# Performance work log

Measured on AMD Instinct MI355X. Metric: run time of the kernel, lower is better.

Reference implementation:

```python
import jax, jax.numpy as jnp
import numpy as np

N = 50000

def gcn_conv(x, W, b, src, dst, n):
    # x: [N, Fin], W: [Fin, Fout]; PyG GCNConv: transform then sym-normalized aggregate (self-loops included in src/dst)
    h = x @ W  # [N, Fout]
    deg = jax.ops.segment_sum(jnp.ones_like(dst, dtype=h.dtype), dst, num_segments=n)
    inv_sqrt = jnp.where(deg > 0, jax.lax.rsqrt(deg), 0.0)
    norm = inv_sqrt[src] * inv_sqrt[dst]  # [E+N]
    msg = h[src] * norm[:, None]
    out = jax.ops.segment_sum(msg, dst, num_segments=n)
    return out + b


def setup_inputs() -> dict:
    key = jax.random.key(0)
    ks = jax.random.split(key, 8)
    d_in, d_h, n_exp, E = 64, 64, 16, 800000
    x = jax.random.normal(ks[0], (N, d_in), dtype=jnp.float32)
    edge_index = jax.random.randint(ks[1], (2, E), 0, N, dtype=jnp.int64)
    s = 1.0 / np.sqrt(d_in)
    W1 = jax.random.uniform(ks[2], (d_in, d_h), minval=-s, maxval=s, dtype=jnp.float32)
    b1 = jnp.zeros((d_h,), jnp.float32)
    W2 = jax.random.uniform(ks[3], (d_h, d_h), minval=-s, maxval=s, dtype=jnp.float32)
    b2 = jnp.zeros((d_h,), jnp.float32)
    Wc = jax.random.uniform(ks[4], (d_h, n_exp), minval=-s, maxval=s, dtype=jnp.float32)
    bc = jnp.zeros((n_exp,), jnp.float32)
    return {"x": x, "edge_index": edge_index, "W1": W1, "b1": b1, "W2": W2, "b2": b2, "Wc": Wc, "bc": bc}


def reference(x, edge_index, W1, b1, W2, b2, Wc, bc):
    # add self-loops once (PyG GCNConv default add_self_loops=True)
    loops = jnp.arange(N, dtype=edge_index.dtype)
    src = jnp.concatenate([edge_index[0], loops])
    dst = jnp.concatenate([edge_index[1], loops])
    h = jax.nn.relu(gcn_conv(x, W1, b1, src, dst, N))
    # dropout is identity in eval mode
    h = jax.nn.relu(gcn_conv(h, W2, b2, src, dst, N))
    return h @ Wc + bc
```

## Files before the change

kernel.cpp:

```cpp
#include <hip/hip_runtime.h>
#include <hip/hip_fp16.h>


#define FDIM 64
#define NCLS 16
#define TILE 2048

__global__ __launch_bounds__(256) void k_histgemm(const int* __restrict__ dst, int E,
                                                  int* __restrict__ H, int nblk,
                                                  const float* __restrict__ X,
                                                  const float* __restrict__ W,
                                                  __half* __restrict__ Yh, int n) {
    __shared__ float Ws[FDIM * FDIM];
    __shared__ int h[256];
    int t = threadIdx.x, blk = blockIdx.x;
    if (blk < nblk) {
        h[t] = 0;
        __syncthreads();
        int i0 = blk * TILE;
#pragma unroll
        for (int k = 0; k < TILE / 256; ++k) {
            int i = i0 + k * 256 + t;
            if (i < E) atomicAdd(&h[dst[i] >> 8], 1);
        }
        __syncthreads();
        H[blk * 256 + t] = h[t];
    } else {
        for (int i = t; i < FDIM * FDIM; i += 256) Ws[i] = W[i];
        __syncthreads();
        int idx = (blk - nblk) * 256 + t;
        int row = idx >> 2;
        int cg = (idx & 3) * 16;
        if (row >= n) return;
        const float4* xr = (const float4*)(X + (size_t)row * FDIM);
        float4 xv[16];
#pragma unroll
        for (int i = 0; i < 16; ++i) xv[i] = xr[i];
        float acc[16];
#pragma unroll
        for (int c = 0; c < 16; ++c) acc[c] = 0.f;
#pragma unroll
        for (int i = 0; i < 16; ++i) {
            float xs[4] = {xv[i].x, xv[i].y, xv[i].z, xv[i].w};
#pragma unroll
            for (int j = 0; j < 4; ++j) {
                float xk = xs[j];
                const float* wr = &Ws[(i * 4 + j) * FDIM + cg];
#pragma unroll
                for (int c = 0; c < 16; ++c) acc[c] += xk * wr[c];
            }
        }
        unsigned u[8];
#pragma unroll
        for (int i = 0; i < 8; ++i) {
            __half2 hp = __floats2half2_rn(acc[2 * i], acc[2 * i + 1]);
            u[i] = *(unsigned*)&hp;
        }
        uint4* yo = (uint4*)(Yh + (size_t)row * FDIM + cg);
        yo[0] = make_uint4(u[0], u[1], u[2], u[3]);
        yo[1] = make_uint4(u[4], u[5], u[6], u[7]);
    }
}

__global__ __launch_bounds__(512) void k_scanH(int* __restrict__ H, int nblk, int* __restrict__ btot) {
    __shared__ int s[512];
    int t = threadIdx.x, b = blockIdx.x;
    int v = (t < nblk) ? H[t * 256 + b] : 0;
    s[t] = v;
    __syncthreads();
    for (int off = 1; off < 512; off <<= 1) {
        int add = (t >= off) ? s[t - off] : 0;
        __syncthreads();
        s[t] += add;
        __syncthreads();
    }
    if (t < nblk) H[t * 256 + b] = s[t] - v;
    if (t == 511) btot[b] = s[511];
}

__global__ __launch_bounds__(256) void k_scatA(const int* __restrict__ src, const int* __restrict__ dst,
                                               int E, const int* __restrict__ H,
                                               const int* __restrict__ btot, int nb,
                                               unsigned* __restrict__ tmp) {
    __shared__ int s[256];
    __shared__ int Hb[256];
    __shared__ int c2[256];
    int t = threadIdx.x, blk = blockIdx.x;
    int v = (t < nb) ? btot[t] : 0;
    s[t] = v;
    __syncthreads();
    for (int off = 1; off < 256; off <<= 1) {
        int add = (t >= off) ? s[t - off] : 0;
        __syncthreads();
        s[t] += add;
        __syncthreads();
    }
    Hb[t] = (s[t] - v) + H[blk * 256 + t];
    c2[t] = 0;
    __syncthreads();
    int i0 = blk * TILE;
#pragma unroll
    for (int k = 0; k < TILE / 256; ++k) {
        int i = i0 + k * 256 + t;
        if (i < E) {
            int sv = src[i], d = dst[i];
            int b = d >> 8;
            unsigned rec = ((unsigned)(d & 255) << 16) | (unsigned)sv;
            int pos = Hb[b] + atomicAdd(&c2[b], 1);
            tmp[pos] = rec;
        }
    }
}

#define COLCAP 8192
__global__ __launch_bounds__(256) void k_binB(const unsigned* __restrict__ tmp,
                                              const int* __restrict__ btot, int nb,
                                              int n, int E, int* __restrict__ row_ptr,
                                              float* __restrict__ inv,
                                              unsigned short* __restrict__ col) {
    __shared__ int dcnt[256], s[256], cur[256];
    __shared__ unsigned short colbuf[COLCAP];
    int t = threadIdx.x, b = blockIdx.x;
    int v = (t < nb) ? btot[t] : 0;
    s[t] = v;
    __syncthreads();
    for (int off = 1; off < 256; off <<= 1) {
        int add = (t >= off) ? s[t - off] : 0;
        __syncthreads();
        s[t] += add;
        __syncthreads();
    }
    __shared__ int baseS;
    if (t == b) baseS = s[t] - v;
    dcnt[t] = 0;
    __syncthreads();
    int base = baseS;
    int cntE = btot[b];
    int node0 = b << 8;
    int nn = min(256, n - node0);
    for (int i = t; i < cntE; i += 256) atomicAdd(&dcnt[tmp[base + i] >> 16], 1);
    __syncthreads();
    int deg = dcnt[t];
    s[t] = deg;
    __syncthreads();
    for (int off = 1; off < 256; off <<= 1) {
        int add = (t >= off) ? s[t - off] : 0;
        __syncthreads();
        s[t] += add;
        __syncthreads();
    }
    int excl = s[t] - deg;
    if (t < nn) {
        row_ptr[node0 + t] = base + excl;
        inv[node0 + t] = rsqrtf((float)(deg + 1));
    }
    if (b == 0 && t == 0) row_ptr[n] = E;
    cur[t] = excl;
    __syncthreads();
    for (int i = t; i < cntE; i += 256) {
        unsigned r = tmp[base + i];
        int pos = atomicAdd(&cur[r >> 16], 1);
        unsigned short vv = (unsigned short)(r & 0xFFFFu);
        if (pos < COLCAP) colbuf[pos] = vv;
        else col[base + pos] = vv;
    }
    __syncthreads();
    int lim = min(cntE, COLCAP);
    for (int i = t; i < lim; i += 256) col[base + i] = colbuf[i];
}

__device__ __forceinline__ void unpack8(const uint4& q, float* f) {
    float2 f0 = __half22float2(*(const __half2*)&q.x);
    float2 f1 = __half22float2(*(const __half2*)&q.y);
    float2 f2 = __half22float2(*(const __half2*)&q.z);
    float2 f3 = __half22float2(*(const __half2*)&q.w);
    f[0] = f0.x; f[1] = f0.y; f[2] = f1.x; f[3] = f1.y;
    f[4] = f2.x; f[5] = f2.y; f[6] = f3.x; f[7] = f3.y;
}

__global__ __launch_bounds__(256) void k_aggF1(const __half* __restrict__ Ph, const float* __restrict__ inv,
                                               const int* __restrict__ row_ptr,
                                               const unsigned short* __restrict__ col,
                                               const float* __restrict__ bias,
                                               const float* __restrict__ W2,
                                               __half* __restrict__ P2, int n) {
    __shared__ float W2s[FDIM * FDIM];
    __shared__ float rbuf[32][FDIM + 1];
    int t = threadIdx.x;
    for (int i = t; i < FDIM * FDIM; i += 256) W2s[i] = W2[i];
    int lane = t & 63;
    int sub = lane >> 3;
    int fl = lane & 7;
    int wid = t >> 6;
    int nl = wid * 8 + sub;
    int node = blockIdx.x * 32 + nl;
    bool alive = node < n;
    int nodeC = alive ? node : (n - 1);
    float iv = inv[nodeC];
    const uint4* Pq = (const uint4*)Ph;
    uint4 selfq = Pq[(size_t)nodeC * 8 + fl];
    float a[8], f[8];
    unpack8(selfq, f);
#pragma unroll
    for (int i = 0; i < 8; ++i) a[i] = iv * f[i];
    int s = row_ptr[nodeC];
    int e = alive ? row_ptr[nodeC + 1] : s;
    for (int j = s; j < e; j += 8) {
        int c[8];
        float wk[8];
        uint4 q[8];
#pragma unroll
        for (int k = 0; k < 8; ++k) {
            int jj = j + k;
            c[k] = col[jj < e ? jj : s];
        }
#pragma unroll
        for (int k = 0; k < 8; ++k) wk[k] = ((j + k) < e) ? inv[c[k]] : 0.f;
#pragma unroll
        for (int k = 0; k < 8; ++k) q[k] = Pq[(size_t)c[k] * 8 + fl];
#pragma unroll
        for (int k = 0; k < 8; ++k) {
            unpack8(q[k], f);
#pragma unroll
            for (int i = 0; i < 8; ++i) a[i] = fmaf(wk[k], f[i], a[i]);
        }
    }
    float4 bb0 = ((const float4*)bias)[fl * 2];
    float4 bb1 = ((const float4*)bias)[fl * 2 + 1];
    float bbv[8] = {bb0.x, bb0.y, bb0.z, bb0.w, bb1.x, bb1.y, bb1.z, bb1.w};
#pragma unroll
    for (int i = 0; i < 8; ++i)
        rbuf[nl][fl * 8 + i] = fmaxf(fmaf(iv, a[i], bbv[i]), 0.f);
    __syncthreads();
    int nl2 = t >> 3;
    int cg = t & 7;
    int node2 = blockIdx.x * 32 + nl2;
    const float* rr = rbuf[nl2];
    float o[8];
#pragma unroll
    for (int i = 0; i < 8; ++i) o[i] = 0.f;
#pragma unroll
    for (int i = 0; i < FDIM; ++i) {
        float xk = rr[i];
        const float* wv = &W2s[i * FDIM + cg * 8];
#pragma unroll
        for (int c = 0; c < 8; ++c) o[c] = fmaf(xk, wv[c], o[c]);
    }
    if (node2 < n) {
        float iv2 = inv[node2];
        unsigned u[4];
#pragma unroll
        for (int i = 0; i < 4; ++i) {
            __half2 hp = __floats2half2_rn(o[2 * i] * iv2, o[2 * i + 1] * iv2);
            u[i] = *(unsigned*)&hp;
        }
        ((uint4*)P2)[(size_t)node2 * 8 + cg] = make_uint4(u[0], u[1], u[2], u[3]);
    }
}

__global__ __launch_bounds__(256) void k_aggF2(const __half* __restrict__ Ph, const float* __restrict__ inv,
                                               const int* __restrict__ row_ptr,
                                               const unsigned short* __restrict__ col,
                                               const float* __restrict__ bias,
                                               const float* __restrict__ Wc, const float* __restrict__ bc,
                                               float* __restrict__ out, int n) {
    __shared__ float WcT[NCLS * FDIM];
    int t = threadIdx.x;
    for (int i = t; i < FDIM * NCLS; i += 256) {
        int c = i & 15, ff = i >> 4;
        WcT[c * FDIM + ff] = Wc[i];
    }
    __syncthreads();
    int lane = t & 63;
    int sub = lane >> 3;
    int fl = lane & 7;
    int wid = t >> 6;
    int node = blockIdx.x * 32 + wid * 8 + sub;
    bool alive = node < n;
    int nodeC = alive ? node : (n - 1);
    float iv = inv[nodeC];
    const uint4* Pq = (const uint4*)Ph;
    uint4 selfq = Pq[(size_t)nodeC * 8 + fl];
    float a[8], f[8];
    unpack8(selfq, a);
    int s = row_ptr[nodeC];
    int e = alive ? row_ptr[nodeC + 1] : s;
    for (int j = s; j < e; j += 8) {
        int c[8];
        float wk[8];
        uint4 q[8];
#pragma unroll
        for (int k = 0; k < 8; ++k) {
            int jj = j + k;
            c[k] = col[jj < e ? jj : s];
            wk[k] = (jj < e) ? 1.f : 0.f;
        }
#pragma unroll
        for (int k = 0; k < 8; ++k) q[k] = Pq[(size_t)c[k] * 8 + fl];
#pragma unroll
        for (int k = 0; k < 8; ++k) {
            unpack8(q[k], f);
#pragma unroll
            for (int i = 0; i < 8; ++i) a[i] = fmaf(wk[k], f[i], a[i]);
        }
    }
    float4 bb0 = ((const float4*)bias)[fl * 2];
    float4 bb1 = ((const float4*)bias)[fl * 2 + 1];
    float bbv[8] = {bb0.x, bb0.y, bb0.z, bb0.w, bb1.x, bb1.y, bb1.z, bb1.w};
    float r[8];
#pragma unroll
    for (int i = 0; i < 8; ++i) r[i] = fmaxf(fmaf(iv, a[i], bbv[i]), 0.f);
    float part[NCLS];
#pragma unroll
    for (int c = 0; c < NCLS; ++c) {
        float4 wv0 = ((const float4*)(WcT + c * FDIM))[fl * 2];
        float4 wv1 = ((const float4*)(WcT + c * FDIM))[fl * 2 + 1];
        part[c] = r[0] * wv0.x;
        part[c] = fmaf(r[1], wv0.y, part[c]);
        part[c] = fmaf(r[2], wv0.z, part[c]);
        part[c] = fmaf(r[3], wv0.w, part[c]);
        part[c] = fmaf(r[4], wv1.x, part[c]);
        part[c] = fmaf(r[5], wv1.y, part[c]);
        part[c] = fmaf(r[6], wv1.z, part[c]);
        part[c] = fmaf(r[7], wv1.w, part[c]);
    }
#pragma unroll
    for (int m = 1; m < 8; m <<= 1) {
#pragma unroll
        for (int c = 0; c < NCLS; ++c) part[c] += __shfl_xor(part[c], m, 64);
    }
    if (alive && fl < 4) {
        float4 bb2 = ((const float4*)bc)[fl];
        float4 o = make_float4(part[fl * 4 + 0] + bb2.x, part[fl * 4 + 1] + bb2.y,
                               part[fl * 4 + 2] + bb2.z, part[fl * 4 + 3] + bb2.w);
        ((float4*)out)[(size_t)node * 4 + fl] = o;
    }
}

static inline size_t align256(size_t x) { return (x + 255) & ~(size_t)255; }

extern "C" void kernel_launch(void* const* d_in, const int* in_sizes, int n_in,
                              void* d_out, int out_size, void* d_ws, size_t ws_size,
                              hipStream_t stream) {
    const float* x  = (const float*)d_in[0];
    const int*   ei = (const int*)d_in[1];
    const float* W1 = (const float*)d_in[2];
    const float* b1 = (const float*)d_in[3];
    const float* W2 = (const float*)d_in[4];
    const float* b2 = (const float*)d_in[5];
    const float* Wc = (const float*)d_in[6];
    const float* bc = (const float*)d_in[7];
    float* out = (float*)d_out;

    const int n = in_sizes[0] / FDIM;
    const int E = in_sizes[1] / 2;
    const int* src = ei;
    const int* dst = ei + E;

    const int nb = (n + 255) >> 8;
    const int nblk = (E + TILE - 1) / TILE;

    char* w = (char*)d_ws;
    size_t off = 0;
    int* H = (int*)(w + off);        off = align256(off + (size_t)nblk * 256 * 4);
    int* btot = (int*)(w + off);     off = align256(off + 256 * 4);
    int* row_ptr = (int*)(w + off);  off = align256(off + (size_t)(n + 1) * 4);
    float* inv = (float*)(w + off);  off = align256(off + (size_t)n * 4);
    unsigned* tmp = (unsigned*)(w + off);             off = align256(off + (size_t)E * 4);
    unsigned short* col = (unsigned short*)(w + off); off = align256(off + (size_t)(E + 8) * 2);
    __half* P1 = (__half*)(w + off); off = align256(off + (size_t)n * FDIM * 2);
    __half* P2 = (__half*)(w + off); off = align256(off + (size_t)n * FDIM * 2);
    (void)ws_size;

    const int nbG = (n * 4 + 255) / 256;
    const int nbA = (n + 31) / 32;

    k_histgemm<<<nblk + nbG, 256, 0, stream>>>(dst, E, H, nblk, x, W1, P1, n);
    k_scanH<<<nb, 512, 0, stream>>>(H, nblk, btot);
    k_scatA<<<nblk, 256, 0, stream>>>(src, dst, E, H, btot, nb, tmp);
    k_binB<<<nb, 256, 0, stream>>>(tmp, btot, nb, n, E, row_ptr, inv, col);

    k_aggF1<<<nbA, 256, 0, stream>>>(P1, inv, row_ptr, col, b1, W2, P2, n);
    k_aggF2<<<nbA, 256, 0, stream>>>(P2, inv, row_ptr, col, b2, Wc, bc, out, n);
}
```

Before: 156.8 us.

## Software-pipeline neighbor gathers in aggregation kernels and widen CSR build blocks to 512

Both aggregation kernels now use a double-buffered loop: the index and feature gathers for the next chunk of eight neighbors are issued before the FMAs on the current chunk, which hides gather latency. The trip count is the maximum degree across the eight nodes sharing a wavefront, so every lane runs the same number of iterations and does masked extra work in place of divergent exits. The scatter and binning kernels that build the CSR structure go from 256 to 512 threads per block, with the 256-wide scans guarded. Gather indexing also drops the size_t cast, which assumes offsets fit in 32 bits, and the doubled buffers raise register pressure.

```diff
diff --git a/kernel.cpp b/kernel.cpp
--- a/kernel.cpp
+++ b/kernel.cpp
@@ -78,7 +78,7 @@
     if (t == 511) btot[b] = s[511];
 }
 
-__global__ __launch_bounds__(256) void k_scatA(const int* __restrict__ src, const int* __restrict__ dst,
+__global__ __launch_bounds__(512) void k_scatA(const int* __restrict__ src, const int* __restrict__ dst,
                                                int E, const int* __restrict__ H,
                                                const int* __restrict__ btot, int nb,
                                                unsigned* __restrict__ tmp) {
@@ -86,22 +86,25 @@
     __shared__ int Hb[256];
     __shared__ int c2[256];
     int t = threadIdx.x, blk = blockIdx.x;
-    int v = (t < nb) ? btot[t] : 0;
-    s[t] = v;
+    int v = 0;
+    if (t < 256) { v = (t < nb) ? btot[t] : 0; s[t] = v; }
     __syncthreads();
     for (int off = 1; off < 256; off <<= 1) {
-        int add = (t >= off) ? s[t - off] : 0;
-        __syncthreads();
-        s[t] += add;
-        __syncthreads();
-    }
-    Hb[t] = (s[t] - v) + H[blk * 256 + t];
-    c2[t] = 0;
+        int add = 0;
+        if (t < 256 && t >= off) add = s[t - off];
+        __syncthreads();
+        if (t < 256) s[t] += add;
+        __syncthreads();
+    }
+    if (t < 256) {
+        Hb[t] = (s[t] - v) + H[blk * 256 + t];
+        c2[t] = 0;
+    }
     __syncthreads();
     int i0 = blk * TILE;
 #pragma unroll
-    for (int k = 0; k < TILE / 256; ++k) {
-        int i = i0 + k * 256 + t;
+    for (int k = 0; k < TILE / 512; ++k) {
+        int i = i0 + k * 512 + t;
         if (i < E) {
             int sv = src[i], d = dst[i];
             int b = d >> 8;
@@ -113,51 +116,53 @@
 }
 
 #define COLCAP 8192
-__global__ __launch_bounds__(256) void k_binB(const unsigned* __restrict__ tmp,
+__global__ __launch_bounds__(512) void k_binB(const unsigned* __restrict__ tmp,
                                               const int* __restrict__ btot, int nb,
                                               int n, int E, int* __restrict__ row_ptr,
                                               float* __restrict__ inv,
                                               unsigned short* __restrict__ col) {
     __shared__ int dcnt[256], s[256], cur[256];
     __shared__ unsigned short colbuf[COLCAP];
+    __shared__ int baseS;
     int t = threadIdx.x, b = blockIdx.x;
-    int v = (t < nb) ? btot[t] : 0;
-    s[t] = v;
+    int v = 0;
+    if (t < 256) { v = (t < nb) ? btot[t] : 0; s[t] = v; }
     __syncthreads();
     for (int off = 1; off < 256; off <<= 1) {
-        int add = (t >= off) ? s[t - off] : 0;
-        __syncthreads();
-        s[t] += add;
-        __syncthreads();
-    }
-    __shared__ int baseS;
+        int add = 0;
+        if (t < 256 && t >= off) add = s[t - off];
+        __syncthreads();
+        if (t < 256) s[t] += add;
+        __syncthreads();
+    }
     if (t == b) baseS = s[t] - v;
-    dcnt[t] = 0;
+    if (t < 256) dcnt[t] = 0;
     __syncthreads();
     int base = baseS;
     int cntE = btot[b];
     int node0 = b << 8;
     int nn = min(256, n - node0);
-    for (int i = t; i < cntE; i += 256) atomicAdd(&dcnt[tmp[base + i] >> 16], 1);
-    __syncthreads();
-    int deg = dcnt[t];
-    s[t] = deg;
+    for (int i = t; i < cntE; i += 512) atomicAdd(&dcnt[tmp[base + i] >> 16], 1);
+    __syncthreads();
+    int deg = 0;
+    if (t < 256) { deg = dcnt[t]; s[t] = deg; }
     __syncthreads();
     for (int off = 1; off < 256; off <<= 1) {
-        int add = (t >= off) ? s[t - off] : 0;
-        __syncthreads();
-        s[t] += add;
-        __syncthreads();
-    }
-    int excl = s[t] - deg;
+        int add = 0;
+        if (t < 256 && t >= off) add = s[t - off];
+        __syncthreads();
+        if (t < 256) s[t] += add;
+        __syncthreads();
+    }
     if (t < nn) {
+        int excl = s[t] - deg;
         row_ptr[node0 + t] = base + excl;
         inv[node0 + t] = rsqrtf((float)(deg + 1));
     }
     if (b == 0 && t == 0) row_ptr[n] = E;
-    cur[t] = excl;
-    __syncthreads();
-    for (int i = t; i < cntE; i += 256) {
+    if (t < 256) cur[t] = s[t] - deg;
+    __syncthreads();
+    for (int i = t; i < cntE; i += 512) {
         unsigned r = tmp[base + i];
         int pos = atomicAdd(&cur[r >> 16], 1);
         unsigned short vv = (unsigned short)(r & 0xFFFFu);
@@ -166,7 +171,7 @@
     }
     __syncthreads();
     int lim = min(cntE, COLCAP);
-    for (int i = t; i < lim; i += 256) col[base + i] = colbuf[i];
+    for (int i = t; i < lim; i += 512) col[base + i] = colbuf[i];
 }
 
 __device__ __forceinline__ void unpack8(const uint4& q, float* f) {
@@ -177,6 +182,59 @@
     f[0] = f0.x; f[1] = f0.y; f[2] = f1.x; f[3] = f1.y;
     f[4] = f2.x; f[5] = f2.y; f[6] = f3.x; f[7] = f3.y;
 }
+__device__ __forceinline__ void load_c(const unsigned short* __restrict__ col,
+                                       int s0, int e, int j, int* c) {
+#pragma unroll
+    for (int k = 0; k < 8; ++k) {
+        int jj = j + k;
+        c[k] = col[jj < e ? jj : s0];
+    }
+}
+__device__ __forceinline__ void load_w(const float* __restrict__ inv, const int* c,
+                                       int e, int j, float* w) {
+#pragma unroll
+    for (int k = 0; k < 8; ++k) w[k] = (j + k < e) ? inv[c[k]] : 0.f;
+}
+__device__ __forceinline__ void mask_w(int e, int j, float* w) {
+#pragma unroll
+    for (int k = 0; k < 8; ++k) w[k] = (j + k < e) ? 1.f : 0.f;
+}
+__device__ __forceinline__ void gatherq(const uint4* __restrict__ Pq, const int* c,
+                                        int fl, uint4* q) {
+#pragma unroll
+    for (int k = 0; k < 8; ++k) q[k] = Pq[c[k] * 8 + fl];
+}
+__device__ __forceinline__ void fma8(const uint4* q, const float* w, float* a) {
+#pragma unroll
+    for (int k = 0; k < 8; ++k) {
+        float f[8];
+        unpack8(q[k], f);
+#pragma unroll
+        for (int i = 0; i < 8; ++i) a[i] = fmaf(w[k], f[i], a[i]);
+    }
+}
+
+#define AGG_PIPE(LOADW_A, LOADW_B)                                            \
+    if (nch > 0) {                                                            \
+        int cA[8], cB[8]; float wA[8], wB[8]; uint4 qA[8], qB[8];             \
+        load_c(col, s0, e, s0, cA);                                           \
+        LOADW_A(s0);                                                          \
+        gatherq(Pq, cA, fl, qA);                                              \
+        if (nch > 1) { load_c(col, s0, e, s0 + 8, cB); LOADW_B(s0 + 8); }     \
+        int t = 0;                                                            \
+        for (;;) {                                                            \
+            if (t + 1 < nch) gatherq(Pq, cB, fl, qB);                         \
+            if (t + 2 < nch) load_c(col, s0, e, s0 + (t + 2) * 8, cA);        \
+            fma8(qA, wA, a);                                                  \
+            if (++t >= nch) break;                                            \
+            if (t + 1 < nch) LOADW_A(s0 + (t + 1) * 8);                       \
+            if (t + 1 < nch) gatherq(Pq, cA, fl, qA);                         \
+            if (t + 2 < nch) load_c(col, s0, e, s0 + (t + 2) * 8, cB);        \
+            fma8(qB, wB, a);                                                  \
+            if (++t >= nch) break;                                            \
+            if (t + 1 < nch) LOADW_B(s0 + (t + 1) * 8);                       \
+        }                                                                     \
+    }
 
 __global__ __launch_bounds__(256) void k_aggF1(const __half* __restrict__ Ph, const float* __restrict__ inv,
                                                const int* __restrict__ row_ptr,
@@ -186,45 +244,35 @@
                                                __half* __restrict__ P2, int n) {
     __shared__ float W2s[FDIM * FDIM];
     __shared__ float rbuf[32][FDIM + 1];
-    int t = threadIdx.x;
-    for (int i = t; i < FDIM * FDIM; i += 256) W2s[i] = W2[i];
-    int lane = t & 63;
+    int t0 = threadIdx.x;
+    for (int i = t0; i < FDIM * FDIM; i += 256) W2s[i] = W2[i];
+    int lane = t0 & 63;
     int sub = lane >> 3;
     int fl = lane & 7;
-    int wid = t >> 6;
+    int wid = t0 >> 6;
     int nl = wid * 8 + sub;
     int node = blockIdx.x * 32 + nl;
     bool alive = node < n;
     int nodeC = alive ? node : (n - 1);
     float iv = inv[nodeC];
     const uint4* Pq = (const uint4*)Ph;
-    uint4 selfq = Pq[(size_t)nodeC * 8 + fl];
+    uint4 selfq = Pq[nodeC * 8 + fl];
     float a[8], f[8];
     unpack8(selfq, f);
 #pragma unroll
     for (int i = 0; i < 8; ++i) a[i] = iv * f[i];
-    int s = row_ptr[nodeC];
-    int e = alive ? row_ptr[nodeC + 1] : s;
-    for (int j = s; j < e; j += 8) {
-        int c[8];
-        float wk[8];
-        uint4 q[8];
-#pragma unroll
-        for (int k = 0; k < 8; ++k) {
-            int jj = j + k;
-            c[k] = col[jj < e ? jj : s];
-        }
-#pragma unroll
-        for (int k = 0; k < 8; ++k) wk[k] = ((j + k) < e) ? inv[c[k]] : 0.f;
-#pragma unroll
-        for (int k = 0; k < 8; ++k) q[k] = Pq[(size_t)c[k] * 8 + fl];
-#pragma unroll
-        for (int k = 0; k < 8; ++k) {
-            unpack8(q[k], f);
-#pragma unroll
-            for (int i = 0; i < 8; ++i) a[i] = fmaf(wk[k], f[i], a[i]);
-        }
-    }
+    int s0 = row_ptr[nodeC];
+    int e = alive ? row_ptr[nodeC + 1] : s0;
+    int dm = e - s0;
+    dm = max(dm, __shfl_xor(dm, 8, 64));
+    dm = max(dm, __shfl_xor(dm, 16, 64));
+    dm = max(dm, __shfl_xor(dm, 32, 64));
+    int nch = (dm + 7) >> 3;
+#define LW_A1(J) load_w(inv, cA, e, (J), wA)
+#define LW_B1(J) load_w(inv, cB, e, (J), wB)
+    AGG_PIPE(LW_A1, LW_B1)
+#undef LW_A1
+#undef LW_B1
     float4 bb0 = ((const float4*)bias)[fl * 2];
     float4 bb1 = ((const float4*)bias)[fl * 2 + 1];
     float bbv[8] = {bb0.x, bb0.y, bb0.z, bb0.w, bb1.x, bb1.y, bb1.z, bb1.w};
@@ -232,8 +280,8 @@
     for (int i = 0; i < 8; ++i)
         rbuf[nl][fl * 8 + i] = fmaxf(fmaf(iv, a[i], bbv[i]), 0.f);
     __syncthreads();
-    int nl2 = t >> 3;
-    int cg = t & 7;
+    int nl2 = t0 >> 3;
+    int cg = t0 & 7;
     int node2 = blockIdx.x * 32 + nl2;
     const float* rr = rbuf[nl2];
     float o[8];
@@ -265,45 +313,36 @@
                                                const float* __restrict__ Wc, const float* __restrict__ bc,
                                                float* __restrict__ out, int n) {
     __shared__ float WcT[NCLS * FDIM];
-    int t = threadIdx.x;
-    for (int i = t; i < FDIM * NCLS; i += 256) {
+    int t0 = threadIdx.x;
+    for (int i = t0; i < FDIM * NCLS; i += 256) {
         int c = i & 15, ff = i >> 4;
         WcT[c * FDIM + ff] = Wc[i];
     }
     __syncthreads();
-    int lane = t & 63;
+    int lane = t0 & 63;
     int sub = lane >> 3;
     int fl = lane & 7;
-    int wid = t >> 6;
+    int wid = t0 >> 6;
     int node = blockIdx.x * 32 + wid * 8 + sub;
     bool alive = node < n;
     int nodeC = alive ? node : (n - 1);
     float iv = inv[nodeC];
     const uint4* Pq = (const uint4*)Ph;
-    uint4 selfq = Pq[(size_t)nodeC * 8 + fl];
+    uint4 selfq = Pq[nodeC * 8 + fl];
     float a[8], f[8];
     unpack8(selfq, a);
-    int s = row_ptr[nodeC];
-    int e = alive ? row_ptr[nodeC + 1] : s;
-    for (int j = s; j < e; j += 8) {
-        int c[8];
-        float wk[8];
-        uint4 q[8];
-#pragma unroll
-        for (int k = 0; k < 8; ++k) {
-            int jj = j + k;
-            c[k] = col[jj < e ? jj : s];
-            wk[k] = (jj < e) ? 1.f : 0.f;
-        }
-#pragma unroll
-        for (int k = 0; k < 8; ++k) q[k] = Pq[(size_t)c[k] * 8 + fl];
-#pragma unroll
-        for (int k = 0; k < 8; ++k) {
-            unpack8(q[k], f);
-#pragma unroll
-            for (int i = 0; i < 8; ++i) a[i] = fmaf(wk[k], f[i], a[i]);
-        }
-    }
+    int s0 = row_ptr[nodeC];
+    int e = alive ? row_ptr[nodeC + 1] : s0;
+    int dm = e - s0;
+    dm = max(dm, __shfl_xor(dm, 8, 64));
+    dm = max(dm, __shfl_xor(dm, 16, 64));
+    dm = max(dm, __shfl_xor(dm, 32, 64));
+    int nch = (dm + 7) >> 3;
+#define LW_A2(J) mask_w(e, (J), wA)
+#define LW_B2(J) mask_w(e, (J), wB)
+    AGG_PIPE(LW_A2, LW_B2)
+#undef LW_A2
+#undef LW_B2
     float4 bb0 = ((const float4*)bias)[fl * 2];
     float4 bb1 = ((const float4*)bias)[fl * 2 + 1];
     float bbv[8] = {bb0.x, bb0.y, bb0.z, bb0.w, bb1.x, bb1.y, bb1.z, bb1.w};
@@ -377,8 +416,8 @@
 
     k_histgemm<<<nblk + nbG, 256, 0, stream>>>(dst, E, H, nblk, x, W1, P1, n);
     k_scanH<<<nb, 512, 0, stream>>>(H, nblk, btot);
-    k_scatA<<<nblk, 256, 0, stream>>>(src, dst, E, H, btot, nb, tmp);
-    k_binB<<<nb, 256, 0, stream>>>(tmp, btot, nb, n, E, row_ptr, inv, col);
+    k_scatA<<<nblk, 512, 0, stream>>>(src, dst, E, H, btot, nb, tmp);
+    k_binB<<<nb, 512, 0, stream>>>(tmp, btot, nb, n, E, row_ptr, inv, col);
 
     k_aggF1<<<nbA, 256, 0, stream>>>(P1, inv, row_ptr, col, b1, W2, P2, n);
     k_aggF2<<<nbA, 256, 0, stream>>>(P2, inv, row_ptr, col, b2, Wc, bc, out, n);
```

After: 190.2 us. +21.4%, slower.

## Sort nodes by degree within each bin to balance aggregation wavefronts

Applied to the files above, without the earlier changes.

The binning kernel now counting-sorts the nodes of each 256-node bin by in-degree and writes a permutation array. The two aggregation kernels process nodes in that permuted order, so the 8 nodes sharing a wavefront have similar edge counts and waste fewer lanes waiting on the longest neighbour loop. The cost is an extra per-block histogram and scan in k_binB, an indirect perm lookup per node, and scattered, less contiguous self-row reads and output writes.

```diff
diff --git a/kernel.cpp b/kernel.cpp
--- a/kernel.cpp
+++ b/kernel.cpp
@@ -117,7 +117,8 @@
                                               const int* __restrict__ btot, int nb,
                                               int n, int E, int* __restrict__ row_ptr,
                                               float* __restrict__ inv,
-                                              unsigned short* __restrict__ col) {
+                                              unsigned short* __restrict__ col,
+                                              int* __restrict__ perm) {
     __shared__ int dcnt[256], s[256], cur[256];
     __shared__ unsigned short colbuf[COLCAP];
     int t = threadIdx.x, b = blockIdx.x;
@@ -167,6 +168,26 @@
     __syncthreads();
     int lim = min(cntE, COLCAP);
     for (int i = t; i < lim; i += 256) col[base + i] = colbuf[i];
+    __syncthreads();
+    s[t] = 0;
+    __syncthreads();
+    int dg = min(deg, 255);
+    if (t < nn) atomicAdd(&s[dg], 1);
+    __syncthreads();
+    int hv = s[t];
+    __syncthreads();
+    for (int off = 1; off < 256; off <<= 1) {
+        int add = (t >= off) ? s[t - off] : 0;
+        __syncthreads();
+        s[t] += add;
+        __syncthreads();
+    }
+    cur[t] = s[t] - hv;
+    __syncthreads();
+    if (t < nn) {
+        int rk = atomicAdd(&cur[dg], 1);
+        perm[node0 + rk] = node0 + t;
+    }
 }
 
 __device__ __forceinline__ void unpack8(const uint4& q, float* f) {
@@ -181,21 +202,22 @@
 __global__ __launch_bounds__(256) void k_aggF1(const __half* __restrict__ Ph, const float* __restrict__ inv,
                                                const int* __restrict__ row_ptr,
                                                const unsigned short* __restrict__ col,
+                                               const int* __restrict__ perm,
                                                const float* __restrict__ bias,
                                                const float* __restrict__ W2,
                                                __half* __restrict__ P2, int n) {
     __shared__ float W2s[FDIM * FDIM];
     __shared__ float rbuf[32][FDIM + 1];
-    int t = threadIdx.x;
-    for (int i = t; i < FDIM * FDIM; i += 256) W2s[i] = W2[i];
-    int lane = t & 63;
+    int t0 = threadIdx.x;
+    for (int i = t0; i < FDIM * FDIM; i += 256) W2s[i] = W2[i];
+    int lane = t0 & 63;
     int sub = lane >> 3;
     int fl = lane & 7;
-    int wid = t >> 6;
+    int wid = t0 >> 6;
     int nl = wid * 8 + sub;
-    int node = blockIdx.x * 32 + nl;
-    bool alive = node < n;
-    int nodeC = alive ? node : (n - 1);
+    int idx = blockIdx.x * 32 + nl;
+    bool alive = idx < n;
+    int nodeC = perm[alive ? idx : (n - 1)];
     float iv = inv[nodeC];
     const uint4* Pq = (const uint4*)Ph;
     uint4 selfq = Pq[(size_t)nodeC * 8 + fl];
@@ -232,9 +254,9 @@
     for (int i = 0; i < 8; ++i)
         rbuf[nl][fl * 8 + i] = fmaxf(fmaf(iv, a[i], bbv[i]), 0.f);
     __syncthreads();
-    int nl2 = t >> 3;
-    int cg = t & 7;
-    int node2 = blockIdx.x * 32 + nl2;
+    int nl2 = t0 >> 3;
+    int cg = t0 & 7;
+    int idx2 = blockIdx.x * 32 + nl2;
     const float* rr = rbuf[nl2];
     float o[8];
 #pragma unroll
@@ -246,7 +268,8 @@
 #pragma unroll
         for (int c = 0; c < 8; ++c) o[c] = fmaf(xk, wv[c], o[c]);
     }
-    if (node2 < n) {
+    if (idx2 < n) {
+        int node2 = perm[idx2];
         float iv2 = inv[node2];
         unsigned u[4];
 #pragma unroll
@@ -261,30 +284,31 @@
 __global__ __launch_bounds__(256) void k_aggF2(const __half* __restrict__ Ph, const float* __restrict__ inv,
                                                const int* __restrict__ row_ptr,
                                                const unsigned short* __restrict__ col,
+                                               const int* __restrict__ perm,
                                                const float* __restrict__ bias,
                                                const float* __restrict__ Wc, const float* __restrict__ bc,
                                                float* __restrict__ out, int n) {
     __shared__ float WcT[NCLS * FDIM];
-    int t = threadIdx.x;
-    for (int i = t; i < FDIM * NCLS; i += 256) {
+    int t0 = threadIdx.x;
+    for (int i = t0; i < FDIM * NCLS; i += 256) {
         int c = i & 15, ff = i >> 4;
         WcT[c * FDIM + ff] = Wc[i];
     }
     __syncthreads();
-    int lane = t & 63;
+    int lane = t0 & 63;
     int sub = lane >> 3;
     int fl = lane & 7;
-    int wid = t >> 6;
-    int node = blockIdx.x * 32 + wid * 8 + sub;
-    bool alive = node < n;
-    int nodeC = alive ? node : (n - 1);
-    float iv = inv[nodeC];
+    int wid = t0 >> 6;
+    int idx = blockIdx.x * 32 + wid * 8 + sub;
+    bool alive = idx < n;
+    int node = perm[alive ? idx : (n - 1)];
+    float iv = inv[node];
     const uint4* Pq = (const uint4*)Ph;
-    uint4 selfq = Pq[(size_t)nodeC * 8 + fl];
+    uint4 selfq = Pq[(size_t)node * 8 + fl];
     float a[8], f[8];
     unpack8(selfq, a);
-    int s = row_ptr[nodeC];
-    int e = alive ? row_ptr[nodeC + 1] : s;
+    int s = row_ptr[node];
+    int e = alive ? row_ptr[node + 1] : s;
     for (int j = s; j < e; j += 8) {
         int c[8];
         float wk[8];
@@ -366,6 +390,7 @@
     int* btot = (int*)(w + off);     off = align256(off + 256 * 4);
     int* row_ptr = (int*)(w + off);  off = align256(off + (size_t)(n + 1) * 4);
     float* inv = (float*)(w + off);  off = align256(off + (size_t)n * 4);
+    int* perm = (int*)(w + off);     off = align256(off + (size_t)n * 4);
     unsigned* tmp = (unsigned*)(w + off);             off = align256(off + (size_t)E * 4);
     unsigned short* col = (unsigned short*)(w + off); off = align256(off + (size_t)(E + 8) * 2);
     __half* P1 = (__half*)(w + off); off = align256(off + (size_t)n * FDIM * 2);
@@ -378,8 +403,8 @@
     k_histgemm<<<nblk + nbG, 256, 0, stream>>>(dst, E, H, nblk, x, W1, P1, n);
     k_scanH<<<nb, 512, 0, stream>>>(H, nblk, btot);
     k_scatA<<<nblk, 256, 0, stream>>>(src, dst, E, H, btot, nb, tmp);
-    k_binB<<<nb, 256, 0, stream>>>(tmp, btot, nb, n, E, row_ptr, inv, col);
-
-    k_aggF1<<<nbA, 256, 0, stream>>>(P1, inv, row_ptr, col, b1, W2, P2, n);
-    k_aggF2<<<nbA, 256, 0, stream>>>(P2, inv, row_ptr, col, b2, Wc, bc, out, n);
-}
+    k_binB<<<nb, 256, 0, stream>>>(tmp, btot, nb, n, E, row_ptr, inv, col, perm);
+
+    k_aggF1<<<nbA, 256, 0, stream>>>(P1, inv, row_ptr, col, perm, b1, W2, P2, n);
+    k_aggF2<<<nbA, 256, 0, stream>>>(P2, inv, row_ptr, col, perm, b2, Wc, bc, out, n);
+}
```

New measurement: 163.1 us. +4.1%, slower.

## Parallelize neighbor gather across edges per wavefront in aggregation kernels

Applied to the files above, without the earlier changes.

Both aggregation kernels now assign one wavefront to each node in turn, eight nodes per wavefront. The 64 lanes are split into 8 edge slots × 8 feature chunks and the partial sums are reduced with cross-lane shuffles. Previously each 8-lane group walked a whole node's edge list serially in batches of eight. Blocks grow to 512 threads and 64 nodes, and the final dense projection is staged through shared memory. The aim is to even out load imbalance from variable degree and expose more memory parallelism, at the cost of shuffle reductions and idle lanes on low-degree nodes.

```diff
diff --git a/kernel.cpp b/kernel.cpp
--- a/kernel.cpp
+++ b/kernel.cpp
@@ -178,63 +178,70 @@
     f[4] = f2.x; f[5] = f2.y; f[6] = f3.x; f[7] = f3.y;
 }
 
-__global__ __launch_bounds__(256) void k_aggF1(const __half* __restrict__ Ph, const float* __restrict__ inv,
+__global__ __launch_bounds__(512) void k_aggF1(const __half* __restrict__ Ph, const float* __restrict__ inv,
                                                const int* __restrict__ row_ptr,
                                                const unsigned short* __restrict__ col,
                                                const float* __restrict__ bias,
                                                const float* __restrict__ W2,
                                                __half* __restrict__ P2, int n) {
     __shared__ float W2s[FDIM * FDIM];
-    __shared__ float rbuf[32][FDIM + 1];
+    __shared__ float rbuf[64][68];
     int t = threadIdx.x;
-    for (int i = t; i < FDIM * FDIM; i += 256) W2s[i] = W2[i];
+    for (int i = t; i < FDIM * FDIM; i += 512) W2s[i] = W2[i];
+    int wid = t >> 6;
     int lane = t & 63;
-    int sub = lane >> 3;
-    int fl = lane & 7;
-    int wid = t >> 6;
-    int nl = wid * 8 + sub;
-    int node = blockIdx.x * 32 + nl;
-    bool alive = node < n;
-    int nodeC = alive ? node : (n - 1);
-    float iv = inv[nodeC];
+    int k = lane >> 3;
+    int f = lane & 7;
+    int node0 = blockIdx.x * 64;
     const uint4* Pq = (const uint4*)Ph;
-    uint4 selfq = Pq[(size_t)nodeC * 8 + fl];
-    float a[8], f[8];
-    unpack8(selfq, f);
-#pragma unroll
-    for (int i = 0; i < 8; ++i) a[i] = iv * f[i];
-    int s = row_ptr[nodeC];
-    int e = alive ? row_ptr[nodeC + 1] : s;
-    for (int j = s; j < e; j += 8) {
-        int c[8];
-        float wk[8];
-        uint4 q[8];
-#pragma unroll
-        for (int k = 0; k < 8; ++k) {
-            int jj = j + k;
-            c[k] = col[jj < e ? jj : s];
-        }
-#pragma unroll
-        for (int k = 0; k < 8; ++k) wk[k] = ((j + k) < e) ? inv[c[k]] : 0.f;
-#pragma unroll
-        for (int k = 0; k < 8; ++k) q[k] = Pq[(size_t)c[k] * 8 + fl];
-#pragma unroll
-        for (int k = 0; k < 8; ++k) {
-            unpack8(q[k], f);
-#pragma unroll
-            for (int i = 0; i < 8; ++i) a[i] = fmaf(wk[k], f[i], a[i]);
-        }
-    }
-    float4 bb0 = ((const float4*)bias)[fl * 2];
-    float4 bb1 = ((const float4*)bias)[fl * 2 + 1];
-    float bbv[8] = {bb0.x, bb0.y, bb0.z, bb0.w, bb1.x, bb1.y, bb1.z, bb1.w};
-#pragma unroll
-    for (int i = 0; i < 8; ++i)
-        rbuf[nl][fl * 8 + i] = fmaxf(fmaf(iv, a[i], bbv[i]), 0.f);
+    for (int it = 0; it < 8; ++it) {
+        int node = node0 + wid * 8 + it;
+        bool alive = node < n;
+        int nodeC = alive ? node : (n - 1);
+        int s = row_ptr[nodeC];
+        int e = alive ? row_ptr[nodeC + 1] : s;
+        float a[8];
+#pragma unroll
+        for (int i = 0; i < 8; ++i) a[i] = 0.f;
+        for (int j = s + k; j < e; j += 8) {
+            int c = col[j];
+            float wk = inv[c];
+            uint4 q = Pq[(size_t)c * 8 + f];
+            float fv[8];
+            unpack8(q, fv);
+#pragma unroll
+            for (int i = 0; i < 8; ++i) a[i] = fmaf(wk, fv[i], a[i]);
+        }
+#pragma unroll
+        for (int m = 8; m < 64; m <<= 1) {
+#pragma unroll
+            for (int i = 0; i < 8; ++i) a[i] += __shfl_xor(a[i], m, 64);
+        }
+        if (k == 0) {
+            float iv = inv[nodeC];
+            uint4 sq = Pq[(size_t)nodeC * 8 + f];
+            float sf[8];
+            unpack8(sq, sf);
+            float4 bb0 = ((const float4*)bias)[f * 2];
+            float4 bb1 = ((const float4*)bias)[f * 2 + 1];
+            float4 r0, r1;
+            r0.x = fmaxf(fmaf(iv, a[0] + iv * sf[0], bb0.x), 0.f);
+            r0.y = fmaxf(fmaf(iv, a[1] + iv * sf[1], bb0.y), 0.f);
+            r0.z = fmaxf(fmaf(iv, a[2] + iv * sf[2], bb0.z), 0.f);
+            r0.w = fmaxf(fmaf(iv, a[3] + iv * sf[3], bb0.w), 0.f);
+            r1.x = fmaxf(fmaf(iv, a[4] + iv * sf[4], bb1.x), 0.f);
+            r1.y = fmaxf(fmaf(iv, a[5] + iv * sf[5], bb1.y), 0.f);
+            r1.z = fmaxf(fmaf(iv, a[6] + iv * sf[6], bb1.z), 0.f);
+            r1.w = fmaxf(fmaf(iv, a[7] + iv * sf[7], bb1.w), 0.f);
+            float4* rw = (float4*)(&rbuf[wid * 8 + it][f * 8]);
+            rw[0] = r0;
+            rw[1] = r1;
+        }
+    }
     __syncthreads();
     int nl2 = t >> 3;
     int cg = t & 7;
-    int node2 = blockIdx.x * 32 + nl2;
+    int node2 = node0 + nl2;
     const float* rr = rbuf[nl2];
     float o[8];
 #pragma unroll
@@ -258,58 +265,76 @@
     }
 }
 
-__global__ __launch_bounds__(256) void k_aggF2(const __half* __restrict__ Ph, const float* __restrict__ inv,
+__global__ __launch_bounds__(512) void k_aggF2(const __half* __restrict__ Ph, const float* __restrict__ inv,
                                                const int* __restrict__ row_ptr,
                                                const unsigned short* __restrict__ col,
                                                const float* __restrict__ bias,
                                                const float* __restrict__ Wc, const float* __restrict__ bc,
                                                float* __restrict__ out, int n) {
     __shared__ float WcT[NCLS * FDIM];
+    __shared__ float rbuf[64][68];
     int t = threadIdx.x;
-    for (int i = t; i < FDIM * NCLS; i += 256) {
+    for (int i = t; i < FDIM * NCLS; i += 512) {
         int c = i & 15, ff = i >> 4;
         WcT[c * FDIM + ff] = Wc[i];
     }
-    __syncthreads();
+    int wid = t >> 6;
     int lane = t & 63;
-    int sub = lane >> 3;
-    int fl = lane & 7;
-    int wid = t >> 6;
-    int node = blockIdx.x * 32 + wid * 8 + sub;
-    bool alive = node < n;
-    int nodeC = alive ? node : (n - 1);
-    float iv = inv[nodeC];
+    int k = lane >> 3;
+    int f = lane & 7;
+    int node0 = blockIdx.x * 64;
     const uint4* Pq = (const uint4*)Ph;
-    uint4 selfq = Pq[(size_t)nodeC * 8 + fl];
-    float a[8], f[8];
-    unpack8(selfq, a);
-    int s = row_ptr[nodeC];
-    int e = alive ? row_ptr[nodeC + 1] : s;
-    for (int j = s; j < e; j += 8) {
-        int c[8];
-        float wk[8];
-        uint4 q[8];
-#pragma unroll
-        for (int k = 0; k < 8; ++k) {
-            int jj = j + k;
-            c[k] = col[jj < e ? jj : s];
-            wk[k] = (jj < e) ? 1.f : 0.f;
-        }
-#pragma unroll
-        for (int k = 0; k < 8; ++k) q[k] = Pq[(size_t)c[k] * 8 + fl];
-#pragma unroll
-        for (int k = 0; k < 8; ++k) {
-            unpack8(q[k], f);
-#pragma unroll
-            for (int i = 0; i < 8; ++i) a[i] = fmaf(wk[k], f[i], a[i]);
-        }
-    }
-    float4 bb0 = ((const float4*)bias)[fl * 2];
-    float4 bb1 = ((const float4*)bias)[fl * 2 + 1];
-    float bbv[8] = {bb0.x, bb0.y, bb0.z, bb0.w, bb1.x, bb1.y, bb1.z, bb1.w};
+    for (int it = 0; it < 8; ++it) {
+        int node = node0 + wid * 8 + it;
+        bool alive = node < n;
+        int nodeC = alive ? node : (n - 1);
+        int s = row_ptr[nodeC];
+        int e = alive ? row_ptr[nodeC + 1] : s;
+        float a[8];
+#pragma unroll
+        for (int i = 0; i < 8; ++i) a[i] = 0.f;
+        for (int j = s + k; j < e; j += 8) {
+            int c = col[j];
+            uint4 q = Pq[(size_t)c * 8 + f];
+            float fv[8];
+            unpack8(q, fv);
+#pragma unroll
+            for (int i = 0; i < 8; ++i) a[i] += fv[i];
+        }
+#pragma unroll
+        for (int m = 8; m < 64; m <<= 1) {
+#pragma unroll
+            for (int i = 0; i < 8; ++i) a[i] += __shfl_xor(a[i], m, 64);
+        }
+        if (k == 0) {
+            float iv = inv[nodeC];
+            uint4 sq = Pq[(size_t)nodeC * 8 + f];
+            float sf[8];
+            unpack8(sq, sf);
+            float4 bb0 = ((const float4*)bias)[f * 2];
+            float4 bb1 = ((const float4*)bias)[f * 2 + 1];
+            float4 r0, r1;
+            r0.x = fmaxf(fmaf(iv, a[0] + sf[0], bb0.x), 0.f);
+            r0.y = fmaxf(fmaf(iv, a[1] + sf[1], bb0.y), 0.f);
+            r0.z = fmaxf(fmaf(iv, a[2] + sf[2], bb0.z), 0.f);
+            r0.w = fmaxf(fmaf(iv, a[3] + sf[3], bb0.w), 0.f);
+            r1.x = fmaxf(fmaf(iv, a[4] + sf[4], bb1.x), 0.f);
+            r1.y = fmaxf(fmaf(iv, a[5] + sf[5], bb1.y), 0.f);
+            r1.z = fmaxf(fmaf(iv, a[6] + sf[6], bb1.z), 0.f);
+            r1.w = fmaxf(fmaf(iv, a[7] + sf[7], bb1.w), 0.f);
+            float4* rw = (float4*)(&rbuf[wid * 8 + it][f * 8]);
+            rw[0] = r0;
+            rw[1] = r1;
+        }
+    }
+    __syncthreads();
+    int nl = t >> 3;
+    int fl = t & 7;
+    int node2 = node0 + nl;
+    const float* rr = rbuf[nl];
     float r[8];
 #pragma unroll
-    for (int i = 0; i < 8; ++i) r[i] = fmaxf(fmaf(iv, a[i], bbv[i]), 0.f);
+    for (int i = 0; i < 8; ++i) r[i] = rr[fl * 8 + i];
     float part[NCLS];
 #pragma unroll
     for (int c = 0; c < NCLS; ++c) {
@@ -329,11 +354,11 @@
 #pragma unroll
         for (int c = 0; c < NCLS; ++c) part[c] += __shfl_xor(part[c], m, 64);
     }
-    if (alive && fl < 4) {
+    if (node2 < n && fl < 4) {
         float4 bb2 = ((const float4*)bc)[fl];
         float4 o = make_float4(part[fl * 4 + 0] + bb2.x, part[fl * 4 + 1] + bb2.y,
                                part[fl * 4 + 2] + bb2.z, part[fl * 4 + 3] + bb2.w);
-        ((float4*)out)[(size_t)node * 4 + fl] = o;
+        ((float4*)out)[(size_t)node2 * 4 + fl] = o;
     }
 }
 
@@ -373,13 +398,13 @@
     (void)ws_size;
 
     const int nbG = (n * 4 + 255) / 256;
-    const int nbA = (n + 31) / 32;
+    const int nbA = (n + 63) / 64;
 
     k_histgemm<<<nblk + nbG, 256, 0, stream>>>(dst, E, H, nblk, x, W1, P1, n);
     k_scanH<<<nb, 512, 0, stream>>>(H, nblk, btot);
     k_scatA<<<nblk, 256, 0, stream>>>(src, dst, E, H, btot, nb, tmp);
     k_binB<<<nb, 256, 0, stream>>>(tmp, btot, nb, n, E, row_ptr, inv, col);
 
-    k_aggF1<<<nbA, 256, 0, stream>>>(P1, inv, row_ptr, col, b1, W2, P2, n);
-    k_aggF2<<<nbA, 256, 0, stream>>>(P2, inv, row_ptr, col, b2, Wc, bc, out, n);
-}
+    k_aggF1<<<nbA, 512, 0, stream>>>(P1, inv, row_ptr, col, b1, W2, P2, n);
+    k_aggF2<<<nbA, 512, 0, stream>>>(P2, inv, row_ptr, col, b2, Wc, bc, out, n);
+}
```

Measured after the change: 183.4 us. 17.0% more time.
